# Optimization experiments

Measured on AMD Instinct MI355X. Metric: run time of the kernel, lower is better.

The kernel has to match this reference:

```python
import jax, jax.numpy as jnp
import numpy as np

B, C, HS, WS = 2, 256, 64, 64
HF, WF = 128, 128
NH = 8
HD = C // NH
K, S, P = 3, 2, 1


def unfold_k3_s2_p1(x):
    # torch nn.Unfold((3,3), stride=2, padding=1): output [B, C*9, L], channel-major
    # ordering idx = c*9 + kh*3 + kw, L row-major over output positions.
    b, c, h, w = x.shape
    xp = jnp.pad(x, ((0, 0), (0, 0), (P, P), (P, P)))
    ho = (h + 2 * P - K) // S + 1
    wo = (w + 2 * P - K) // S + 1
    parts = [xp[:, :, kh:kh + S * (ho - 1) + 1:S, kw:kw + S * (wo - 1) + 1:S]
             for kh in range(K) for kw in range(K)]
    patches = jnp.stack(parts, axis=2)  # [B, C, 9, ho, wo]
    return patches.reshape(b, c * K * K, ho * wo)


def setup_inputs() -> dict:
    key = jax.random.key(0)
    ks = jax.random.split(key, 7)
    w_scale = jnp.float32(0.02)
    return {
        "feat": jax.random.normal(ks[0], (B, C, HF, WF), dtype=jnp.float32),
        "src": jax.random.normal(ks[1], (B, C, HS, WS), dtype=jnp.float32),
        "Wq": jax.random.normal(ks[2], (C, C), dtype=jnp.float32) * w_scale,
        "bq": jnp.zeros((C,), dtype=jnp.float32),
        "Wk": jax.random.normal(ks[3], (C, C), dtype=jnp.float32) * w_scale,
        "bk": jnp.zeros((C,), dtype=jnp.float32),
        "Wv": jax.random.normal(ks[4], (C, C), dtype=jnp.float32) * w_scale,
        "bv": jnp.zeros((C,), dtype=jnp.float32),
        "Wo": jax.random.normal(ks[5], (C, C), dtype=jnp.float32) * w_scale,
        "bo": jnp.zeros((C,), dtype=jnp.float32),
    }


def reference(feat, src, Wq, bq, Wk, bk, Wv, bv, Wo, bo):
    b, c, h, w = src.shape
    # query: 1x1 unfold == flatten spatial -> [B, Lq, C]
    query = src.reshape(b, c, h * w).transpose(0, 2, 1)
    # key/value: 3x3 im2col of feat, then keep only FIRST c entries of the C*9 dim
    kv = unfold_k3_s2_p1(feat).transpose(0, 2, 1)[..., :c]  # [B, Lkv, C]
    # MultiheadAttention (batch_first), embed_dim=C, 8 heads
    q = query @ Wq.T + bq
    k = kv @ Wk.T + bk
    v = kv @ Wv.T + bv

    def split_heads(x):
        return x.reshape(b, -1, NH, HD).transpose(0, 2, 1, 3)  # [B, H, L, D]

    qh, kh_, vh = split_heads(q), split_heads(k), split_heads(v)
    scale = jnp.float32(1.0 / np.sqrt(HD))
    scores = jnp.einsum('bhqd,bhkd->bhqk', qh, kh_) * scale
    attn = jax.nn.softmax(scores, axis=-1)
    oh = jnp.einsum('bhqk,bhkd->bhqd', attn, vh)
    o = oh.transpose(0, 2, 1, 3).reshape(b, -1, c)
    o = o @ Wo.T + bo  # out projection
    # fold with kernel (1,1) == reshape back to [B, C, h, w]
    out = o.transpose(0, 2, 1).reshape(b, c, h, w)
    return out * src
```

## Files before the change

kernel.cpp:

```cpp
#include <hip/hip_runtime.h>
#include <math.h>

#define B_  2
#define C_  256
#define NH_ 8
#define HD_ 32
#define L_  4096
#define M_  (B_*L_)

typedef __attribute__((ext_vector_type(8))) short bf16x8;
typedef __attribute__((ext_vector_type(4))) float f32x4;

__device__ __forceinline__ unsigned short f2bf(float x) {
    unsigned u = __float_as_uint(x);
    unsigned r = u + 0x7fffu + ((u >> 16) & 1u);
    return (unsigned short)(r >> 16);
}

#define GLOAD_LDS16(gp, lp) \
    __builtin_amdgcn_global_load_lds( \
        (const __attribute__((address_space(1))) void*)(gp), \
        (__attribute__((address_space(3))) void*)(lp), 16, 0, 0)

__global__ __launch_bounds__(256) void build_kv_kernel(
    const float* __restrict__ feat, float* __restrict__ kv)
{
    int idx = blockIdx.x * 256 + threadIdx.x;
    int j = idx & (C_ - 1);
    int l = (idx >> 8) & (L_ - 1);
    int b = idx >> 20;
    int c  = j / 9;
    int r  = j - c * 9;
    int kh = r / 3;
    int kw = r - kh * 3;
    int oh = l >> 6, ow = l & 63;
    int h = 2 * oh + kh - 1;
    int w = 2 * ow + kw - 1;
    float val = 0.0f;
    if ((unsigned)h < 128u && (unsigned)w < 128u)
        val = feat[((size_t)(b * C_ + c) * 128 + h) * 128 + w];
    kv[idx] = val;
}

template <bool TRANS_A, int OMODE>
__global__ __launch_bounds__(256) void gemm_kernel(
    const float* __restrict__ A, const float* __restrict__ W,
    const float* __restrict__ bias, void* __restrict__ out,
    const float* __restrict__ src)
{
    __shared__ float As[32][68];
    __shared__ float Ws[32][68];

    const int m0 = blockIdx.x * 64;
    const int n0 = blockIdx.y * 64;
    const int t  = threadIdx.x;
    const int tm = t >> 4;
    const int tn = t & 15;

    float acc[4][4] = {};

    for (int k0 = 0; k0 < C_; k0 += 32) {
        if (!TRANS_A) {
            #pragma unroll
            for (int u = t; u < 512; u += 256) {
                int row = u >> 3, c4 = u & 7;
                float4 val = *(const float4*)(A + (size_t)(m0 + row) * C_ + k0 + c4 * 4);
                As[c4 * 4 + 0][row] = val.x;
                As[c4 * 4 + 1][row] = val.y;
                As[c4 * 4 + 2][row] = val.z;
                As[c4 * 4 + 3][row] = val.w;
            }
        } else {
            int b  = m0 >> 12;
            int l0 = m0 & (L_ - 1);
            #pragma unroll
            for (int u = t; u < 512; u += 256) {
                int c = u >> 4, l4 = u & 15;
                float4 val = *(const float4*)(A + (size_t)b * C_ * L_ +
                                              (size_t)(k0 + c) * L_ + l0 + l4 * 4);
                *(float4*)&As[c][l4 * 4] = val;
            }
        }
        #pragma unroll
        for (int u = t; u < 512; u += 256) {
            int row = u >> 3, c4 = u & 7;
            float4 val = *(const float4*)(W + (size_t)(n0 + row) * C_ + k0 + c4 * 4);
            Ws[c4 * 4 + 0][row] = val.x;
            Ws[c4 * 4 + 1][row] = val.y;
            Ws[c4 * 4 + 2][row] = val.z;
            Ws[c4 * 4 + 3][row] = val.w;
        }
        __syncthreads();
        #pragma unroll
        for (int kk = 0; kk < 32; kk++) {
            float4 a4 = *(float4*)&As[kk][tm * 4];
            float4 w4 = *(float4*)&Ws[kk][tn * 4];
            float a[4] = {a4.x, a4.y, a4.z, a4.w};
            float w[4] = {w4.x, w4.y, w4.z, w4.w};
            #pragma unroll
            for (int i = 0; i < 4; i++)
                #pragma unroll
                for (int jj = 0; jj < 4; jj++)
                    acc[i][jj] += a[i] * w[jj];
        }
        __syncthreads();
    }

    if (OMODE == 1) {
        unsigned short* o = (unsigned short*)out;
        #pragma unroll
        for (int i = 0; i < 4; i++) {
            int m = m0 + tm * 4 + i;
            int n = n0 + tn * 4;
            ushort4 pk = make_ushort4(
                f2bf(acc[i][0] + bias[n + 0]), f2bf(acc[i][1] + bias[n + 1]),
                f2bf(acc[i][2] + bias[n + 2]), f2bf(acc[i][3] + bias[n + 3]));
            *(ushort4*)(o + ((size_t)m << 8) + n) = pk;
        }
    } else if (OMODE == 2) {
        unsigned short* o = (unsigned short*)out;
        int b = m0 >> 12;
        int key = (m0 & (L_ - 1)) + tm * 4;
        #pragma unroll
        for (int jj = 0; jj < 4; jj++) {
            int n = n0 + tn * 4 + jj;
            float bb = bias[n];
            ushort4 pk = make_ushort4(
                f2bf(acc[0][jj] + bb), f2bf(acc[1][jj] + bb),
                f2bf(acc[2][jj] + bb), f2bf(acc[3][jj] + bb));
            *(ushort4*)(o + ((size_t)(b * 256 + n) << 12) + key) = pk;
        }
    } else {
        float* o = (float*)out;
        #pragma unroll
        for (int i = 0; i < 4; i++) {
            int m = m0 + tm * 4 + i;
            int b = m >> 12, l = m & (L_ - 1);
            #pragma unroll
            for (int jj = 0; jj < 4; jj++) {
                int n = n0 + tn * 4 + jj;
                float val = acc[i][jj] + bias[n];
                size_t oidx = (size_t)(b * C_ + n) * L_ + l;
                o[oidx] = val * src[oidx];
            }
        }
    }
}

__global__ __launch_bounds__(256) void attn_mfma_kernel(
    const unsigned short* __restrict__ qbf,
    const unsigned short* __restrict__ kbf,
    const unsigned short* __restrict__ vbf,
    float* __restrict__ ob)
{
    __shared__ __align__(16) char Ksh[4096];
    __shared__ __align__(16) char Vsh[4096];

    const int id   = blockIdx.x;
    const int xcd  = id & 7;
    const int slot = id >> 3;
    const int bh   = xcd + 8 * (slot >> 6);
    const int qt   = slot & 63;
    const int b = bh >> 3, h = bh & 7;

    const int t    = threadIdx.x;
    const int w    = t >> 6;
    const int lane = t & 63;
    const int lg   = lane >> 4;
    const int lc   = lane & 15;

    const int qrow = qt * 64 + w * 16 + lc;
    const bf16x8 qf = *(const bf16x8*)(qbf + ((size_t)(b * L_ + qrow) << 8) + h * 32 + (lg << 3));

    const char* kg = (const char*)kbf + ((size_t)(b * L_ + w * 16 + lc) << 9) + h * 64 + (lg << 4);
    const int vmt = t >> 7, vks = (t >> 6) & 1;
    const char* vg = (const char*)vbf + ((size_t)(b * 256 + h * 32 + vmt * 16 + lc) << 13)
                     + ((vks * 32 + (lg << 3)) << 1);

    f32x4 oacc[2];
    oacc[0] = (f32x4){0.f, 0.f, 0.f, 0.f};
    oacc[1] = (f32x4){0.f, 0.f, 0.f, 0.f};
    float mrun = -INFINITY, lrun = 0.0f;
    const float scale = 0.17677669529663687f;
    const f32x4 zero4 = (f32x4){0.f, 0.f, 0.f, 0.f};

    for (int kt = 0; kt < 64; kt++) {
        __syncthreads();
        GLOAD_LDS16(kg + (size_t)kt * 32768, Ksh + t * 16);
        GLOAD_LDS16(vg + (size_t)kt * 128,   Vsh + t * 16);
        __syncthreads();

        f32x4 sa[4];
        #pragma unroll
        for (int f = 0; f < 4; f++) {
            bf16x8 kf = *(const bf16x8*)(Ksh + f * 1024 + lane * 16);
            sa[f] = __builtin_amdgcn_mfma_f32_16x16x32_bf16(kf, qf, zero4, 0, 0, 0);
        }

        float sv[16];
        float tmax = -INFINITY;
        #pragma unroll
        for (int f = 0; f < 4; f++)
            #pragma unroll
            for (int i = 0; i < 4; i++) {
                float x = sa[f][i] * scale;
                sv[f * 4 + i] = x;
                tmax = fmaxf(tmax, x);
            }
        tmax = fmaxf(tmax, __shfl_xor(tmax, 16));
        tmax = fmaxf(tmax, __shfl_xor(tmax, 32));
        float mnew   = fmaxf(mrun, tmax);
        float factor = __expf(mrun - mnew);
        float pv[16];
        float ps = 0.f;
        #pragma unroll
        for (int j2 = 0; j2 < 16; j2++) {
            float p = __expf(sv[j2] - mnew);
            pv[j2] = p;
            ps += p;
        }
        ps += __shfl_xor(ps, 16);
        ps += __shfl_xor(ps, 32);
        lrun = lrun * factor + ps;
        mrun = mnew;
        #pragma unroll
        for (int i = 0; i < 4; i++) { oacc[0][i] *= factor; oacc[1][i] *= factor; }

        unsigned W8[8];
        #pragma unroll
        for (int f = 0; f < 4; f++)
            #pragma unroll
            for (int m2 = 0; m2 < 2; m2++)
                W8[f * 2 + m2] = (unsigned)f2bf(pv[f * 4 + 2 * m2])
                               | ((unsigned)f2bf(pv[f * 4 + 2 * m2 + 1]) << 16);

        #pragma unroll
        for (int ks = 0; ks < 2; ks++) {
            union { unsigned u[4]; bf16x8 v; } bu;
            #pragma unroll
            for (int j = 0; j < 4; j++) {
                int srcl = lc + 16 * ((lg & 1) * 2 + (j >> 1));
                unsigned va = (unsigned)__shfl((int)W8[(ks * 2) * 2 + (j & 1)], srcl);
                unsigned vb = (unsigned)__shfl((int)W8[(ks * 2 + 1) * 2 + (j & 1)], srcl);
                bu.u[j] = (lg >= 2) ? vb : va;
            }
            bf16x8 v0 = *(const bf16x8*)(Vsh + 0 * 2048 + ks * 1024 + lane * 16);
            bf16x8 v1 = *(const bf16x8*)(Vsh + 1 * 2048 + ks * 1024 + lane * 16);
            oacc[0] = __builtin_amdgcn_mfma_f32_16x16x32_bf16(v0, bu.v, oacc[0], 0, 0, 0);
            oacc[1] = __builtin_amdgcn_mfma_f32_16x16x32_bf16(v1, bu.v, oacc[1], 0, 0, 0);
        }
    }

    float invl = 1.0f / lrun;
    #pragma unroll
    for (int mt = 0; mt < 2; mt++) {
        f32x4 ov = oacc[mt] * invl;
        *(f32x4*)(ob + ((size_t)(b * L_ + qrow) << 8) + h * 32 + mt * 16 + (lg << 2)) = ov;
    }
}

extern "C" void kernel_launch(void* const* d_in, const int* in_sizes, int n_in,
                              void* d_out, int out_size, void* d_ws, size_t ws_size,
                              hipStream_t stream)
{
    const float* feat = (const float*)d_in[0];
    const float* src  = (const float*)d_in[1];
    const float* Wq   = (const float*)d_in[2];
    const float* bq   = (const float*)d_in[3];
    const float* Wk   = (const float*)d_in[4];
    const float* bk   = (const float*)d_in[5];
    const float* Wv   = (const float*)d_in[6];
    const float* bv   = (const float*)d_in[7];
    const float* Wo   = (const float*)d_in[8];
    const float* bo   = (const float*)d_in[9];
    float* out = (float*)d_out;

    float* ws = (float*)d_ws;
    const size_t NE = (size_t)M_ * C_;
    float* kv = ws;
    float* ob = ws + NE;
    unsigned short* qbf = (unsigned short*)(ws + 2 * NE);
    unsigned short* kbf = qbf + NE;
    unsigned short* vbf = kbf + NE;

    build_kv_kernel<<<(B_ * L_ * C_) / 256, 256, 0, stream>>>(feat, kv);

    dim3 ggrid(M_ / 64, C_ / 64);
    gemm_kernel<true,  1><<<ggrid, 256, 0, stream>>>(src, Wq, bq, qbf, nullptr);
    gemm_kernel<false, 1><<<ggrid, 256, 0, stream>>>(kv,  Wk, bk, kbf, nullptr);
    gemm_kernel<false, 2><<<ggrid, 256, 0, stream>>>(kv,  Wv, bv, vbf, nullptr);

    attn_mfma_kernel<<<1024, 256, 0, stream>>>(qbf, kbf, vbf, ob);

    gemm_kernel<false, 3><<<ggrid, 256, 0, stream>>>(ob, Wo, bo, out, src);
}
```

Measured before the change: 317.6 us.

## Split attention keys across two block halves and fold softmax scale into Q

The attention kernel now runs 512 threads per block. Each half processes half of the key sequence with its own LDS buffers, and the two partial softmax states (max, sum, output) are merged through shared memory at the end. This doubles the waves per query tile to hide the serialized load-sync-compute loop latency. Separately, the 1/sqrt(d)·log2(e) factor is folded into the Q projection output so the inner loop uses exp2 without a per-score multiply. In exchange, the kernel needs more LDS, adds a final merge step, and rounds the pre-scaled Q to bf16.

New measurement: 320.7 us. About the same (+1.0%).

```diff
diff --git a/kernel.cpp b/kernel.cpp
--- a/kernel.cpp
+++ b/kernel.cpp
@@ -46,7 +46,7 @@
 __global__ __launch_bounds__(256) void gemm_kernel(
     const float* __restrict__ A, const float* __restrict__ W,
     const float* __restrict__ bias, void* __restrict__ out,
-    const float* __restrict__ src)
+    const float* __restrict__ src, float oscale)
 {
     __shared__ float As[32][68];
     __shared__ float Ws[32][68];
@@ -113,8 +113,10 @@
             int m = m0 + tm * 4 + i;
             int n = n0 + tn * 4;
             ushort4 pk = make_ushort4(
-                f2bf(acc[i][0] + bias[n + 0]), f2bf(acc[i][1] + bias[n + 1]),
-                f2bf(acc[i][2] + bias[n + 2]), f2bf(acc[i][3] + bias[n + 3]));
+                f2bf((acc[i][0] + bias[n + 0]) * oscale),
+                f2bf((acc[i][1] + bias[n + 1]) * oscale),
+                f2bf((acc[i][2] + bias[n + 2]) * oscale),
+                f2bf((acc[i][3] + bias[n + 3]) * oscale));
             *(ushort4*)(o + ((size_t)m << 8) + n) = pk;
         }
     } else if (OMODE == 2) {
@@ -147,14 +149,15 @@
     }
 }
 
-__global__ __launch_bounds__(256) void attn_mfma_kernel(
+__global__ __launch_bounds__(512) void attn_mfma_kernel(
     const unsigned short* __restrict__ qbf,
     const unsigned short* __restrict__ kbf,
     const unsigned short* __restrict__ vbf,
     float* __restrict__ ob)
 {
-    __shared__ __align__(16) char Ksh[4096];
-    __shared__ __align__(16) char Vsh[4096];
+    __shared__ __align__(16) char Ksh[2][4096];
+    __shared__ __align__(16) char Vsh[2][4096];
+    __shared__ float mb[4][64][11];
 
     const int id   = blockIdx.x;
     const int xcd  = id & 7;
@@ -163,59 +166,67 @@
     const int qt   = slot & 63;
     const int b = bh >> 3, h = bh & 7;
 
-    const int t    = threadIdx.x;
-    const int w    = t >> 6;
-    const int lane = t & 63;
-    const int lg   = lane >> 4;
-    const int lc   = lane & 15;
-
-    const int qrow = qt * 64 + w * 16 + lc;
+    const int t      = threadIdx.x;
+    const int lane   = t & 63;
+    const int wl     = (t >> 6) & 3;
+    const int halfid = t >> 8;
+    const int th     = t & 255;
+    const int lg     = lane >> 4;
+    const int lc     = lane & 15;
+
+    const int qrow = qt * 64 + wl * 16 + lc;
     const bf16x8 qf = *(const bf16x8*)(qbf + ((size_t)(b * L_ + qrow) << 8) + h * 32 + (lg << 3));
 
-    const char* kg = (const char*)kbf + ((size_t)(b * L_ + w * 16 + lc) << 9) + h * 64 + (lg << 4);
-    const int vmt = t >> 7, vks = (t >> 6) & 1;
-    const char* vg = (const char*)vbf + ((size_t)(b * 256 + h * 32 + vmt * 16 + lc) << 13)
-                     + ((vks * 32 + (lg << 3)) << 1);
+    const char* kg = (const char*)kbf
+        + ((size_t)(b * L_ + halfid * 2048 + wl * 16 + lc) << 9) + h * 64 + (lg << 4);
+    const int vmt = (t >> 7) & 1, vks = wl & 1;
+    const char* vg = (const char*)vbf
+        + ((size_t)(b * 256 + h * 32 + vmt * 16 + lc) << 13)
+        + ((size_t)(halfid * 2048 + vks * 32 + (lg << 3)) << 1);
+    char* kdst = Ksh[halfid] + th * 16;
+    char* vdst = Vsh[halfid] + th * 16;
+    const char* kbase = Ksh[halfid];
+    const char* vbase = Vsh[halfid];
 
     f32x4 oacc[2];
     oacc[0] = (f32x4){0.f, 0.f, 0.f, 0.f};
     oacc[1] = (f32x4){0.f, 0.f, 0.f, 0.f};
     float mrun = -INFINITY, lrun = 0.0f;
-    const float scale = 0.17677669529663687f;
     const f32x4 zero4 = (f32x4){0.f, 0.f, 0.f, 0.f};
 
-    for (int kt = 0; kt < 64; kt++) {
+    for (int kt = 0; kt < 32; kt++) {
         __syncthreads();
-        GLOAD_LDS16(kg + (size_t)kt * 32768, Ksh + t * 16);
-        GLOAD_LDS16(vg + (size_t)kt * 128,   Vsh + t * 16);
+        GLOAD_LDS16(kg + (size_t)kt * 32768, kdst);
+        GLOAD_LDS16(vg + (size_t)kt * 128,   vdst);
         __syncthreads();
 
         f32x4 sa[4];
         #pragma unroll
         for (int f = 0; f < 4; f++) {
-            bf16x8 kf = *(const bf16x8*)(Ksh + f * 1024 + lane * 16);
+            bf16x8 kf = *(const bf16x8*)(kbase + f * 1024 + lane * 16);
             sa[f] = __builtin_amdgcn_mfma_f32_16x16x32_bf16(kf, qf, zero4, 0, 0, 0);
         }
 
         float sv[16];
-        float tmax = -INFINITY;
         #pragma unroll
         for (int f = 0; f < 4; f++)
             #pragma unroll
-            for (int i = 0; i < 4; i++) {
-                float x = sa[f][i] * scale;
-                sv[f * 4 + i] = x;
-                tmax = fmaxf(tmax, x);
-            }
+            for (int i = 0; i < 4; i++)
+                sv[f * 4 + i] = sa[f][i];
+        float t0 = fmaxf(fmaxf(sv[0], sv[1]),  fmaxf(sv[2], sv[3]));
+        float t1 = fmaxf(fmaxf(sv[4], sv[5]),  fmaxf(sv[6], sv[7]));
+        float t2 = fmaxf(fmaxf(sv[8], sv[9]),  fmaxf(sv[10], sv[11]));
+        float t3 = fmaxf(fmaxf(sv[12], sv[13]), fmaxf(sv[14], sv[15]));
+        float tmax = fmaxf(fmaxf(t0, t1), fmaxf(t2, t3));
         tmax = fmaxf(tmax, __shfl_xor(tmax, 16));
         tmax = fmaxf(tmax, __shfl_xor(tmax, 32));
         float mnew   = fmaxf(mrun, tmax);
-        float factor = __expf(mrun - mnew);
+        float factor = exp2f(mrun - mnew);
         float pv[16];
         float ps = 0.f;
         #pragma unroll
         for (int j2 = 0; j2 < 16; j2++) {
-            float p = __expf(sv[j2] - mnew);
+            float p = exp2f(sv[j2] - mnew);
             pv[j2] = p;
             ps += p;
         }
@@ -244,18 +255,36 @@
                 unsigned vb = (unsigned)__shfl((int)W8[(ks * 2 + 1) * 2 + (j & 1)], srcl);
                 bu.u[j] = (lg >= 2) ? vb : va;
             }
-            bf16x8 v0 = *(const bf16x8*)(Vsh + 0 * 2048 + ks * 1024 + lane * 16);
-            bf16x8 v1 = *(const bf16x8*)(Vsh + 1 * 2048 + ks * 1024 + lane * 16);
+            bf16x8 v0 = *(const bf16x8*)(vbase + 0 * 2048 + ks * 1024 + lane * 16);
+            bf16x8 v1 = *(const bf16x8*)(vbase + 1 * 2048 + ks * 1024 + lane * 16);
             oacc[0] = __builtin_amdgcn_mfma_f32_16x16x32_bf16(v0, bu.v, oacc[0], 0, 0, 0);
             oacc[1] = __builtin_amdgcn_mfma_f32_16x16x32_bf16(v1, bu.v, oacc[1], 0, 0, 0);
         }
     }
 
-    float invl = 1.0f / lrun;
-    #pragma unroll
-    for (int mt = 0; mt < 2; mt++) {
-        f32x4 ov = oacc[mt] * invl;
-        *(f32x4*)(ob + ((size_t)(b * L_ + qrow) << 8) + h * 32 + mt * 16 + (lg << 2)) = ov;
+    __syncthreads();
+    if (halfid == 1) {
+        float* s = &mb[wl][lane][0];
+        #pragma unroll
+        for (int i = 0; i < 4; i++) { s[i] = oacc[0][i]; s[4 + i] = oacc[1][i]; }
+        s[8] = mrun; s[9] = lrun;
+    }
+    __syncthreads();
+    if (halfid == 0) {
+        const float* s = &mb[wl][lane][0];
+        float m1 = s[8], l1 = s[9];
+        float mF = fmaxf(mrun, m1);
+        float f0 = exp2f(mrun - mF);
+        float f1 = exp2f(m1 - mF);
+        float invl = 1.0f / (lrun * f0 + l1 * f1);
+        #pragma unroll
+        for (int mt = 0; mt < 2; mt++) {
+            f32x4 ov;
+            #pragma unroll
+            for (int i = 0; i < 4; i++)
+                ov[i] = (oacc[mt][i] * f0 + s[mt * 4 + i] * f1) * invl;
+            *(f32x4*)(ob + ((size_t)(b * L_ + qrow) << 8) + h * 32 + mt * 16 + (lg << 2)) = ov;
+        }
     }
 }
 
@@ -285,12 +314,14 @@
 
     build_kv_kernel<<<(B_ * L_ * C_) / 256, 256, 0, stream>>>(feat, kv);
 
+    const float qscale = 0.17677669529663687f * 1.4426950408889634f;
+
     dim3 ggrid(M_ / 64, C_ / 64);
-    gemm_kernel<true,  1><<<ggrid, 256, 0, stream>>>(src, Wq, bq, qbf, nullptr);
-    gemm_kernel<false, 1><<<ggrid, 256, 0, stream>>>(kv,  Wk, bk, kbf, nullptr);
-    gemm_kernel<false, 2><<<ggrid, 256, 0, stream>>>(kv,  Wv, bv, vbf, nullptr);
-
-    attn_mfma_kernel<<<1024, 256, 0, stream>>>(qbf, kbf, vbf, ob);
-
-    gemm_kernel<false, 3><<<ggrid, 256, 0, stream>>>(ob, Wo, bo, out, src);
-}
+    gemm_kernel<true,  1><<<ggrid, 256, 0, stream>>>(src, Wq, bq, qbf, nullptr, qscale);
+    gemm_kernel<false, 1><<<ggrid, 256, 0, stream>>>(kv,  Wk, bk, kbf, nullptr, 1.0f);
+    gemm_kernel<false, 2><<<ggrid, 256, 0, stream>>>(kv,  Wv, bv, vbf, nullptr, 1.0f);
+
+    attn_mfma_kernel<<<1024, 512, 0, stream>>>(qbf, kbf, vbf, ob);
+
+    gemm_kernel<false, 3><<<ggrid, 256, 0, stream>>>(ob, Wo, bo, out, src, 1.0f);
+}
```
